# Optimization experiments

Measured on AMD Instinct MI355X. Metric: run time of the kernel, lower is better.

## Reference

```python
import jax, jax.numpy as jnp
import numpy as np

N = 50000          # nodes
E = 800000         # edges
IN_C = 128
HID = 64
NUM_GRAPHS = 256
OUT_C = 8


def setup_inputs() -> dict:
    key = jax.random.key(0)
    k1, k2, k3, k4, k5, k6, k7 = jax.random.split(key, 7)
    x = jax.random.normal(k1, (N, IN_C), dtype=jnp.float32)
    edge_index = jax.random.randint(k2, (2, E), 0, N, dtype=jnp.int64)
    batch = jnp.sort(jax.random.randint(k3, (N,), 0, NUM_GRAPHS, dtype=jnp.int64))
    # GCNConv params (lin: in->hid, glorot-ish) and fc params (hid->8)
    W = jax.random.normal(k4, (IN_C, HID), dtype=jnp.float32) / np.sqrt(IN_C)
    b = jnp.zeros((HID,), dtype=jnp.float32)
    Wfc = jax.random.normal(k5, (HID, OUT_C), dtype=jnp.float32) / np.sqrt(HID)
    bfc = jnp.zeros((OUT_C,), dtype=jnp.float32)
    return {"x": x, "edge_index": edge_index, "batch": batch,
            "W": W, "b": b, "Wfc": Wfc, "bfc": bfc}


def reference(x, edge_index, batch, W, b, Wfc, bfc):
    n = x.shape[0]
    # GCNConv: linear transform first, then normalized propagation w/ self-loops
    x_lin = x @ W                                             # [N, HID]
    self_loops = jnp.arange(n, dtype=edge_index.dtype)
    row = jnp.concatenate([edge_index[0], self_loops])        # src
    col = jnp.concatenate([edge_index[1], self_loops])        # dst
    # symmetric normalization: deg over destinations (weight = 1)
    deg = jax.ops.segment_sum(jnp.ones_like(col, dtype=x.dtype), col,
                              num_segments=n)                 # [N]
    dinv = jnp.where(deg > 0, jax.lax.rsqrt(deg), 0.0)
    norm = dinv[row] * dinv[col]                              # [E+N]
    msg = x_lin[row] * norm[:, None]                          # gather + scale
    h = jax.ops.segment_sum(msg, col, num_segments=n) + b     # scatter-add
    h = jax.nn.relu(h)
    # global_mean_pool over batch ids
    sums = jax.ops.segment_sum(h, batch, num_segments=NUM_GRAPHS)
    cnts = jax.ops.segment_sum(jnp.ones((n,), dtype=x.dtype), batch,
                               num_segments=NUM_GRAPHS)
    pooled = sums / jnp.maximum(cnts, 1.0)[:, None]           # [G, HID]
    return pooled @ Wfc + bfc                                 # [G, 8]
```

## Files before the change

### kernel.cpp

```cpp
#include <hip/hip_runtime.h>
#include <stdint.h>

#define N_NODES 50000
#define N_EDGES 800000
#define IN_C    128
#define HID     64
#define NUM_G   256
#define OUT_C   8

#define NBH   64
#define ES    (N_EDGES / NBH)
#define NBIN  50048
#define NPK   (NBIN / 2)

#define NQ_H   4
#define BINS_H (NBIN / NQ_H)
#define PK_H   (BINS_H / 2)
#define NQ_S   8
#define BINS_S (NBIN / NQ_S)

#define NBLK_CSR 98

__device__ __forceinline__ void gload_lds16(const void* g, void* l) {
    __builtin_amdgcn_global_load_lds(
        (const __attribute__((address_space(1))) unsigned int*)g,
        (__attribute__((address_space(3))) unsigned int*)l, 16, 0, 0);
}

__device__ __forceinline__ unsigned short f2bf(float f) {
    union { float f; unsigned u; } v; v.f = f;
    unsigned r = v.u + 0x7fff + ((v.u >> 16) & 1);
    return (unsigned short)(r >> 16);
}
__device__ __forceinline__ float bf2f(unsigned short u) {
    union { unsigned u; float f; } v; v.u = ((unsigned)u) << 16;
    return v.f;
}

__global__ __launch_bounds__(256) void k_histB(const int* __restrict__ col,
                                               int* __restrict__ part,
                                               int* __restrict__ doneCnt) {
    __shared__ int lh[PK_H];
    const int tid = threadIdx.x;
    if (blockIdx.x == 0 && tid == 0)
        __hip_atomic_store(doneCnt, 0, __ATOMIC_RELAXED, __HIP_MEMORY_SCOPE_AGENT);
    const int r = blockIdx.x >> 2;
    const int q = blockIdx.x & 3;
    const int q0 = q * BINS_H;
    for (int i = tid; i < PK_H; i += 256) lh[i] = 0;
    __syncthreads();
    const int4* col4 = (const int4*)(col + r * ES);
#pragma unroll 2
    for (int j4 = tid; j4 < ES / 4; j4 += 256) {
        int4 c = col4[j4];
        unsigned d0 = (unsigned)(c.x - q0), d1 = (unsigned)(c.y - q0);
        unsigned d2 = (unsigned)(c.z - q0), d3 = (unsigned)(c.w - q0);
        if (d0 < BINS_H) atomicAdd(&lh[d0 >> 1], 1 << ((d0 & 1) * 16));
        if (d1 < BINS_H) atomicAdd(&lh[d1 >> 1], 1 << ((d1 & 1) * 16));
        if (d2 < BINS_H) atomicAdd(&lh[d2 >> 1], 1 << ((d2 & 1) * 16));
        if (d3 < BINS_H) atomicAdd(&lh[d3 >> 1], 1 << ((d3 & 1) * 16));
    }
    __syncthreads();
    int* dst = part + r * NPK + q * PK_H;
    for (int i = tid; i < PK_H; i += 256) dst[i] = lh[i];
}

__global__ __launch_bounds__(256) void k_csr(int* __restrict__ part,
                                             float* __restrict__ dinv,
                                             int* __restrict__ nstart,
                                             const int* __restrict__ batch,
                                             int* __restrict__ gstart,
                                             float* __restrict__ pooled,
                                             int* __restrict__ agg,
                                             int* __restrict__ doneCnt) {
    __shared__ int sScan[256];
    __shared__ int sAgg[NBLK_CSR];
    __shared__ int sPrefix;
    const int tid = threadIdx.x;
    const int b   = blockIdx.x;
    const int t   = b * 256 + tid;
    const bool valid = t < NPK;

    int s0 = 0, s1 = 0;
    if (valid) {
        int idx = t;
#pragma unroll 4
        for (int r = 0; r < NBH; ++r, idx += NPK) {
            int v = part[idx];
            part[idx] = s0 | (s1 << 16);
            s0 += v & 0xffff;
            s1 += (v >> 16) & 0xffff;
        }
        ((float2*)dinv)[t] = make_float2(rsqrtf((float)(s0 + 1)),
                                         rsqrtf((float)(s1 + 1)));
    }

    int ps = s0 + s1;
    sScan[tid] = ps;
    __syncthreads();
    int acc = ps;
#pragma unroll
    for (int off = 1; off < 256; off <<= 1) {
        int tv = (tid >= off) ? sScan[tid - off] : 0;
        __syncthreads();
        acc += tv;
        sScan[tid] = acc;
        __syncthreads();
    }
    const int excl  = acc - ps;
    const int total = sScan[255];

    if (tid == 0) {
        __hip_atomic_store(&agg[b], total, __ATOMIC_RELAXED, __HIP_MEMORY_SCOPE_AGENT);
        __hip_atomic_fetch_add(doneCnt, 1, __ATOMIC_RELEASE, __HIP_MEMORY_SCOPE_AGENT);
        while (__hip_atomic_load(doneCnt, __ATOMIC_ACQUIRE, __HIP_MEMORY_SCOPE_AGENT) < NBLK_CSR)
            __builtin_amdgcn_s_sleep(1);
    }
    __syncthreads();
    if (tid < NBLK_CSR)
        sAgg[tid] = __hip_atomic_load(&agg[tid], __ATOMIC_RELAXED, __HIP_MEMORY_SCOPE_AGENT);
    __syncthreads();
    if (tid == 0) {
        int p = 0;
        for (int j = 0; j < b; ++j) p += sAgg[j];
        sPrefix = p;
    }
    __syncthreads();

    if (valid) {
        int base = sPrefix + excl;
        ((int2*)nstart)[t] = make_int2(base, base + s0);
    }
    if (t <= NUM_G) {
        int lo = 0, hi = N_NODES;
        while (lo < hi) {
            int mid = (lo + hi) >> 1;
            if (batch[mid] < t) lo = mid + 1; else hi = mid;
        }
        gstart[t] = lo;
    }
    if (t < NUM_G * HID) pooled[t] = 0.f;
}

__global__ __launch_bounds__(256) void k_scat2(const int* __restrict__ row,
                                               const int* __restrict__ col,
                                               const int* __restrict__ part,
                                               const int* __restrict__ nstart,
                                               int* __restrict__ ed) {
    __shared__ int lc[BINS_S];
    const int tid = threadIdx.x;
    const int r = blockIdx.x >> 3;
    const int q = blockIdx.x & 7;
    const int q0 = q * BINS_S;
    for (int i = tid; i < BINS_S; i += 256) {
        int bin = q0 + i;
        int bb = part[r * NPK + (bin >> 1)];
        int off = (i & 1) ? ((bb >> 16) & 0xffff) : (bb & 0xffff);
        lc[i] = nstart[bin] + off;
    }
    __syncthreads();
    const int4* col4 = (const int4*)(col + r * ES);
    const int4* row4 = (const int4*)(row + r * ES);
#pragma unroll 2
    for (int j4 = tid; j4 < ES / 4; j4 += 256) {
        int4 c = col4[j4];
        int4 s = row4[j4];
        unsigned d0 = (unsigned)(c.x - q0), d1 = (unsigned)(c.y - q0);
        unsigned d2 = (unsigned)(c.z - q0), d3 = (unsigned)(c.w - q0);
        if (d0 < BINS_S) ed[atomicAdd(&lc[d0], 1)] = s.x;
        if (d1 < BINS_S) ed[atomicAdd(&lc[d1], 1)] = s.y;
        if (d2 < BINS_S) ed[atomicAdd(&lc[d2], 1)] = s.z;
        if (d3 < BINS_S) ed[atomicAdd(&lc[d3], 1)] = s.w;
    }
}

__global__ __launch_bounds__(256) void k_lin(const float* __restrict__ x,
                                             const float* __restrict__ W,
                                             const float* __restrict__ dinv,
                                             unsigned short* __restrict__ yb) {
    __shared__ float xs[64 * IN_C];
    __shared__ float Ws[IN_C * HID];
    const int tid = threadIdx.x;
    const size_t row0 = (size_t)blockIdx.x * 64;
    const int ln = tid & 63, wv = tid >> 6;

    {
        const char* wsrc = (const char*)W;
#pragma unroll
        for (int it = 0; it < 8; ++it) {
            int c = wv * 8 + it;
            gload_lds16(wsrc + c * 1024 + ln * 16, (char*)Ws + c * 1024);
        }
    }
    if (row0 + 64 <= N_NODES) {
        const char* gsrc = (const char*)(x + row0 * IN_C);
#pragma unroll
        for (int it = 0; it < 8; ++it) {
            int c = wv * 8 + it;
            gload_lds16(gsrc + c * 1024 + ln * 16, (char*)xs + c * 1024);
        }
    } else {
        const float4* src = (const float4*)(x + row0 * IN_C);
        for (int i4 = tid; i4 < 2048; i4 += 256) {
            int r = i4 >> 5;
            float4 v = make_float4(0.f, 0.f, 0.f, 0.f);
            if (row0 + r < N_NODES) v = src[i4];
            ((float4*)xs)[i4] = v;
        }
    }
    __syncthreads();

    const int ty = tid >> 4, tx = tid & 15;
    const int r0 = ty * 4, c0 = tx * 4;
    float acc[4][4] = {};

#define AC(ai, kk) ((kk)==0 ? av##ai.x : (kk)==1 ? av##ai.y : (kk)==2 ? av##ai.z : av##ai.w)
#define ROWF(ai, kk, bv) \
    acc[ai][0] = fmaf(AC(ai,kk), bv.x, acc[ai][0]); \
    acc[ai][1] = fmaf(AC(ai,kk), bv.y, acc[ai][1]); \
    acc[ai][2] = fmaf(AC(ai,kk), bv.z, acc[ai][2]); \
    acc[ai][3] = fmaf(AC(ai,kk), bv.w, acc[ai][3]);
#define K4(kk, bv) ROWF(0,kk,bv) ROWF(1,kk,bv) ROWF(2,kk,bv) ROWF(3,kk,bv)

    for (int k = 0; k < IN_C; k += 4) {
        float4 av0 = *(const float4*)&xs[(r0+0)*IN_C + k];
        float4 av1 = *(const float4*)&xs[(r0+1)*IN_C + k];
        float4 av2 = *(const float4*)&xs[(r0+2)*IN_C + k];
        float4 av3 = *(const float4*)&xs[(r0+3)*IN_C + k];
        float4 bv0 = *(const float4*)&Ws[(k+0)*HID + c0];
        float4 bv1 = *(const float4*)&Ws[(k+1)*HID + c0];
        float4 bv2 = *(const float4*)&Ws[(k+2)*HID + c0];
        float4 bv3 = *(const float4*)&Ws[(k+3)*HID + c0];
        K4(0, bv0) K4(1, bv1) K4(2, bv2) K4(3, bv3)
    }
#undef K4
#undef ROWF
#undef AC

#pragma unroll
    for (int i = 0; i < 4; ++i) {
        size_t r = row0 + r0 + i;
        if (r < N_NODES) {
            float dv = dinv[r];
            ushort4 o;
            o.x = f2bf(acc[i][0] * dv);
            o.y = f2bf(acc[i][1] * dv);
            o.z = f2bf(acc[i][2] * dv);
            o.w = f2bf(acc[i][3] * dv);
            *(ushort4*)&yb[r * HID + c0] = o;
        }
    }
}

#define NPT 8
__global__ __launch_bounds__(256) void k_gpool(const int* __restrict__ ed,
                                               const int* __restrict__ nstart,
                                               const float* __restrict__ dinv,
                                               const unsigned short* __restrict__ yb,
                                               const int* __restrict__ batch,
                                               const float* __restrict__ bias,
                                               float* __restrict__ pooled) {
    const int lane  = threadIdx.x & 63;
    const int node0 = (blockIdx.x * 4 + (threadIdx.x >> 6)) * NPT;
    if (node0 >= N_NODES) return;
    const float bsv = bias[lane];
    float pacc = 0.f;
    int   cur  = -1;
#pragma unroll 1
    for (int t0 = 0; t0 < NPT; ++t0) {
        int node = node0 + t0;
        if (node >= N_NODES) break;
        const int n0 = nstart[node], n1 = nstart[node + 1];
        float acc = bf2f(yb[(size_t)node * HID + lane]);
        int t = n0;
        for (; t + 8 <= n1; t += 8) {
            int s0 = __builtin_amdgcn_readfirstlane(ed[t]);
            int s1 = __builtin_amdgcn_readfirstlane(ed[t+1]);
            int s2 = __builtin_amdgcn_readfirstlane(ed[t+2]);
            int s3 = __builtin_amdgcn_readfirstlane(ed[t+3]);
            int s4 = __builtin_amdgcn_readfirstlane(ed[t+4]);
            int s5 = __builtin_amdgcn_readfirstlane(ed[t+5]);
            int s6 = __builtin_amdgcn_readfirstlane(ed[t+6]);
            int s7 = __builtin_amdgcn_readfirstlane(ed[t+7]);
            float v0 = bf2f(yb[(size_t)s0 * HID + lane]);
            float v1 = bf2f(yb[(size_t)s1 * HID + lane]);
            float v2 = bf2f(yb[(size_t)s2 * HID + lane]);
            float v3 = bf2f(yb[(size_t)s3 * HID + lane]);
            float v4 = bf2f(yb[(size_t)s4 * HID + lane]);
            float v5 = bf2f(yb[(size_t)s5 * HID + lane]);
            float v6 = bf2f(yb[(size_t)s6 * HID + lane]);
            float v7 = bf2f(yb[(size_t)s7 * HID + lane]);
            acc += ((v0 + v1) + (v2 + v3)) + ((v4 + v5) + (v6 + v7));
        }
        for (; t + 4 <= n1; t += 4) {
            int s0 = __builtin_amdgcn_readfirstlane(ed[t]);
            int s1 = __builtin_amdgcn_readfirstlane(ed[t+1]);
            int s2 = __builtin_amdgcn_readfirstlane(ed[t+2]);
            int s3 = __builtin_amdgcn_readfirstlane(ed[t+3]);
            float v0 = bf2f(yb[(size_t)s0 * HID + lane]);
            float v1 = bf2f(yb[(size_t)s1 * HID + lane]);
            float v2 = bf2f(yb[(size_t)s2 * HID + lane]);
            float v3 = bf2f(yb[(size_t)s3 * HID + lane]);
            acc += (v0 + v1) + (v2 + v3);
        }
        for (; t < n1; ++t) {
            int s = __builtin_amdgcn_readfirstlane(ed[t]);
            acc += bf2f(yb[(size_t)s * HID + lane]);
        }
        float hv = fmaxf(acc * dinv[node] + bsv, 0.f);
        int bg = batch[node];
        if (bg != cur) {
            if (cur >= 0) atomicAdd(&pooled[cur * HID + lane], pacc);
            cur  = bg;
            pacc = hv;
        } else {
            pacc += hv;
        }
    }
    if (cur >= 0) atomicAdd(&pooled[cur * HID + lane], pacc);
}

__global__ void k_out(const float* __restrict__ pooled, const int* __restrict__ gstart,
                      const float* __restrict__ Wfc, const float* __restrict__ bfc,
                      float* __restrict__ out) {
    int idx = blockIdx.x * blockDim.x + threadIdx.x;
    int g = idx >> 3;
    int o = idx & 7;
    float inv = 1.f / fmaxf((float)(gstart[g + 1] - gstart[g]), 1.f);
    float acc = 0.f;
#pragma unroll
    for (int k = 0; k < HID; ++k) acc += pooled[g * HID + k] * Wfc[k * OUT_C + o];
    out[idx] = acc * inv + bfc[o];
}

extern "C" void kernel_launch(void* const* d_in, const int* in_sizes, int n_in,
                              void* d_out, int out_size, void* d_ws, size_t ws_size,
                              hipStream_t stream) {
    const float* x     = (const float*)d_in[0];
    const int*   eidx  = (const int*)d_in[1];
    const int*   batch = (const int*)d_in[2];
    const float* W     = (const float*)d_in[3];
    const float* b     = (const float*)d_in[4];
    const float* Wfc   = (const float*)d_in[5];
    const float* bfc   = (const float*)d_in[6];
    float*       out   = (float*)d_out;

    const int* row = eidx;
    const int* col = eidx + N_EDGES;

    char* p = (char*)d_ws;
    int*            part = (int*)p;
    unsigned short* yb   = (unsigned short*)p;
    p += (size_t)NBH * NPK * 4;
    float* dinv   = (float*)p;  p += (size_t)NBIN * 4;
    float* pooled = (float*)p;  p += (size_t)NUM_G * HID * 4;
    int*   nstart = (int*)p;    p += (size_t)(NBIN + 4) * 4;
    int*   gstart = (int*)p;    p += 1040;
    int*   agg    = (int*)p;    p += 400;
    int*   doneCnt= (int*)p;    p += 16;
    int*   ed     = (int*)p;

    k_histB <<<NBH * NQ_H, 256, 0, stream>>>(col, part, doneCnt);
    k_csr   <<<NBLK_CSR, 256, 0, stream>>>(part, dinv, nstart, batch, gstart, pooled, agg, doneCnt);
    k_scat2 <<<NBH * NQ_S, 256, 0, stream>>>(row, col, part, nstart, ed);
    k_lin   <<<(N_NODES + 63) / 64, 256, 0, stream>>>(x, W, dinv, yb);
    k_gpool <<<(N_NODES + 4 * NPT - 1) / (4 * NPT), 256, 0, stream>>>(ed, nstart, dinv, yb, batch, b, pooled);
    k_out   <<<8, 256, 0, stream>>>(pooled, gstart, Wfc, bfc, out);
}
```

Measured before the change: 104.9 us.

## Split wave into four 16-lane edge groups with vectorized bf16x4 gathers

The gather-pool kernel now gives each wave four groups of 16 lanes. Each group handles a different edge of the node's CSR list and loads four bf16 features per lane as one 8-byte load, where before one edge was read at a time as a 2-byte load per lane. Partial sums from the groups are combined with cross-lane shuffles, and only group 0 issues the atomic adds into the pooled output. This aims to raise memory-level parallelism and cut per-edge instruction and readfirstlane overhead, at the cost of shuffle reductions and masked tail iterations for nodes of low degree.

```diff
diff --git a/kernel.cpp b/kernel.cpp
--- a/kernel.cpp
+++ b/kernel.cpp
@@ -32,9 +32,14 @@
     unsigned r = v.u + 0x7fff + ((v.u >> 16) & 1);
     return (unsigned short)(r >> 16);
 }
-__device__ __forceinline__ float bf2f(unsigned short u) {
-    union { unsigned u; float f; } v; v.u = ((unsigned)u) << 16;
-    return v.f;
+
+__device__ __forceinline__ float4 bf4(uint2 u) {
+    union { unsigned u; float f; } a, b, c, d;
+    a.u = u.x << 16;
+    b.u = u.x & 0xffff0000u;
+    c.u = u.y << 16;
+    d.u = u.y & 0xffff0000u;
+    return make_float4(a.f, b.f, c.f, d.f);
 }
 
 __global__ __launch_bounds__(256) void k_histB(const int* __restrict__ col,
@@ -260,64 +265,82 @@
                                                const int* __restrict__ batch,
                                                const float* __restrict__ bias,
                                                float* __restrict__ pooled) {
-    const int lane  = threadIdx.x & 63;
+    const int lane = threadIdx.x & 63;
+    const int grp  = lane >> 4;
+    const int sl   = lane & 15;
     const int node0 = (blockIdx.x * 4 + (threadIdx.x >> 6)) * NPT;
     if (node0 >= N_NODES) return;
-    const float bsv = bias[lane];
-    float pacc = 0.f;
-    int   cur  = -1;
+    const float4 b4 = *(const float4*)&bias[4 * sl];
+    float4 pacc = make_float4(0.f, 0.f, 0.f, 0.f);
+    int    cur  = -1;
 #pragma unroll 1
     for (int t0 = 0; t0 < NPT; ++t0) {
         int node = node0 + t0;
         if (node >= N_NODES) break;
         const int n0 = nstart[node], n1 = nstart[node + 1];
-        float acc = bf2f(yb[(size_t)node * HID + lane]);
-        int t = n0;
-        for (; t + 8 <= n1; t += 8) {
-            int s0 = __builtin_amdgcn_readfirstlane(ed[t]);
-            int s1 = __builtin_amdgcn_readfirstlane(ed[t+1]);
-            int s2 = __builtin_amdgcn_readfirstlane(ed[t+2]);
-            int s3 = __builtin_amdgcn_readfirstlane(ed[t+3]);
-            int s4 = __builtin_amdgcn_readfirstlane(ed[t+4]);
-            int s5 = __builtin_amdgcn_readfirstlane(ed[t+5]);
-            int s6 = __builtin_amdgcn_readfirstlane(ed[t+6]);
-            int s7 = __builtin_amdgcn_readfirstlane(ed[t+7]);
-            float v0 = bf2f(yb[(size_t)s0 * HID + lane]);
-            float v1 = bf2f(yb[(size_t)s1 * HID + lane]);
-            float v2 = bf2f(yb[(size_t)s2 * HID + lane]);
-            float v3 = bf2f(yb[(size_t)s3 * HID + lane]);
-            float v4 = bf2f(yb[(size_t)s4 * HID + lane]);
-            float v5 = bf2f(yb[(size_t)s5 * HID + lane]);
-            float v6 = bf2f(yb[(size_t)s6 * HID + lane]);
-            float v7 = bf2f(yb[(size_t)s7 * HID + lane]);
-            acc += ((v0 + v1) + (v2 + v3)) + ((v4 + v5) + (v6 + v7));
-        }
-        for (; t + 4 <= n1; t += 4) {
-            int s0 = __builtin_amdgcn_readfirstlane(ed[t]);
-            int s1 = __builtin_amdgcn_readfirstlane(ed[t+1]);
-            int s2 = __builtin_amdgcn_readfirstlane(ed[t+2]);
-            int s3 = __builtin_amdgcn_readfirstlane(ed[t+3]);
-            float v0 = bf2f(yb[(size_t)s0 * HID + lane]);
-            float v1 = bf2f(yb[(size_t)s1 * HID + lane]);
-            float v2 = bf2f(yb[(size_t)s2 * HID + lane]);
-            float v3 = bf2f(yb[(size_t)s3 * HID + lane]);
-            acc += (v0 + v1) + (v2 + v3);
-        }
-        for (; t < n1; ++t) {
-            int s = __builtin_amdgcn_readfirstlane(ed[t]);
-            acc += bf2f(yb[(size_t)s * HID + lane]);
-        }
-        float hv = fmaxf(acc * dinv[node] + bsv, 0.f);
+        float4 facc = make_float4(0.f, 0.f, 0.f, 0.f);
+        int t = n0 + grp;
+        const int nfull8 = n0 + ((n1 - n0) & ~7);
+#pragma unroll 1
+        for (; t < nfull8; t += 8) {
+            int srcA = ed[t];
+            int srcB = ed[t + 4];
+            uint2 ua = *(const uint2*)&yb[(size_t)srcA * HID + 4 * sl];
+            uint2 ub = *(const uint2*)&yb[(size_t)srcB * HID + 4 * sl];
+            float4 va = bf4(ua), vb = bf4(ub);
+            facc.x += va.x + vb.x;
+            facc.y += va.y + vb.y;
+            facc.z += va.z + vb.z;
+            facc.w += va.w + vb.w;
+        }
+#pragma unroll
+        for (int step = 0; step < 2; ++step) {
+            bool act = t < n1;
+            int tt = act ? t : 0;
+            int src = ed[tt];
+            uint2 u = *(const uint2*)&yb[(size_t)src * HID + 4 * sl];
+            if (act) {
+                float4 v = bf4(u);
+                facc.x += v.x; facc.y += v.y; facc.z += v.z; facc.w += v.w;
+            }
+            t += 4;
+        }
+        facc.x += __shfl_xor(facc.x, 16, 64);
+        facc.y += __shfl_xor(facc.y, 16, 64);
+        facc.z += __shfl_xor(facc.z, 16, 64);
+        facc.w += __shfl_xor(facc.w, 16, 64);
+        facc.x += __shfl_xor(facc.x, 32, 64);
+        facc.y += __shfl_xor(facc.y, 32, 64);
+        facc.z += __shfl_xor(facc.z, 32, 64);
+        facc.w += __shfl_xor(facc.w, 32, 64);
+        uint2 us = *(const uint2*)&yb[(size_t)node * HID + 4 * sl];
+        float4 vs = bf4(us);
+        float dv = dinv[node];
+        float4 hv;
+        hv.x = fmaxf((facc.x + vs.x) * dv + b4.x, 0.f);
+        hv.y = fmaxf((facc.y + vs.y) * dv + b4.y, 0.f);
+        hv.z = fmaxf((facc.z + vs.z) * dv + b4.z, 0.f);
+        hv.w = fmaxf((facc.w + vs.w) * dv + b4.w, 0.f);
         int bg = batch[node];
         if (bg != cur) {
-            if (cur >= 0) atomicAdd(&pooled[cur * HID + lane], pacc);
+            if (cur >= 0 && grp == 0) {
+                atomicAdd(&pooled[cur * HID + 4 * sl + 0], pacc.x);
+                atomicAdd(&pooled[cur * HID + 4 * sl + 1], pacc.y);
+                atomicAdd(&pooled[cur * HID + 4 * sl + 2], pacc.z);
+                atomicAdd(&pooled[cur * HID + 4 * sl + 3], pacc.w);
+            }
             cur  = bg;
             pacc = hv;
         } else {
-            pacc += hv;
-        }
-    }
-    if (cur >= 0) atomicAdd(&pooled[cur * HID + lane], pacc);
+            pacc.x += hv.x; pacc.y += hv.y; pacc.z += hv.z; pacc.w += hv.w;
+        }
+    }
+    if (cur >= 0 && grp == 0) {
+        atomicAdd(&pooled[cur * HID + 4 * sl + 0], pacc.x);
+        atomicAdd(&pooled[cur * HID + 4 * sl + 1], pacc.y);
+        atomicAdd(&pooled[cur * HID + 4 * sl + 2], pacc.z);
+        atomicAdd(&pooled[cur * HID + 4 * sl + 3], pacc.w);
+    }
 }
 
 __global__ void k_out(const float* __restrict__ pooled, const int* __restrict__ gstart,
```

Measured after the change: 102.3 us. 2.5% less time.
